# Kernel tuning notes

Measured on AMD Instinct MI355X. Metric: run time of the kernel, lower is better.

The kernel has to match this reference:

```python
import jax, jax.numpy as jnp
import numpy as np

N_HEADS = 32
N_KV_HEADS = 8


def _rope(x, cos, sin):
    # x: [B, S, H, D]; cos/sin: [S, D//2]; complex multiply on consecutive pairs
    B, S, H, D = x.shape
    xr = x.reshape(B, S, H, D // 2, 2)
    x0, x1 = xr[..., 0], xr[..., 1]
    c = cos[None, :, None, :]
    s = sin[None, :, None, :]
    o0 = x0 * c - x1 * s
    o1 = x0 * s + x1 * c
    return jnp.stack([o0, o1], axis=-1).reshape(B, S, H, D)


def setup_inputs():
    key = jax.random.key(0)
    ks = jax.random.split(key, 5)
    B, S, D = 1, 2048, 2048
    hd = D // N_HEADS  # 64
    x = jax.random.normal(ks[0], (B, S, D), jnp.float32)
    wq = jax.random.normal(ks[1], (D, D), jnp.float32) * 0.02
    wk = jax.random.normal(ks[2], (D, N_KV_HEADS * hd), jnp.float32) * 0.02
    wv = jax.random.normal(ks[3], (D, N_KV_HEADS * hd), jnp.float32) * 0.02
    wo = jax.random.normal(ks[4], (D, D), jnp.float32) * 0.02
    # true rotary frequencies (theta_cis = exp(i * pos * freq)), shape [S, hd//2]
    pos = jnp.arange(S, dtype=jnp.float32)
    freqs = 1.0 / (10000.0 ** (jnp.arange(0, hd, 2, dtype=jnp.float32) / hd))
    ang = pos[:, None] * freqs[None, :]
    return {"x": x, "theta_cos": jnp.cos(ang), "theta_sin": jnp.sin(ang),
            "wq": wq, "wk": wk, "wv": wv, "wo": wo}


def reference(x, theta_cos, theta_sin, wq, wk, wv, wo):
    B, S, D = x.shape
    hd = D // N_HEADS
    rep = N_HEADS // N_KV_HEADS
    xq = (x @ wq).reshape(B, S, N_HEADS, hd)
    # NOTE: module applies RoPE to K and V (not Q) - reproduced faithfully
    xk = _rope((x @ wk).reshape(B, S, N_KV_HEADS, hd), theta_cos, theta_sin)
    xv = _rope((x @ wv).reshape(B, S, N_KV_HEADS, hd), theta_cos, theta_sin)
    # GQA: repeat_interleave kv heads along head dim
    xk = jnp.repeat(xk, rep, axis=2)
    xv = jnp.repeat(xv, rep, axis=2)
    att = jnp.einsum('bqhd,bkhd->bhqk', xq, xk) * (hd ** -0.5)
    # faithful to torch.tril + masked_fill(att == 0.0, -inf)
    att = jnp.tril(att)
    att = jnp.where(att == 0.0, -jnp.inf, att)
    att = jax.nn.softmax(att, axis=-1)
    y = jnp.einsum('bhqk,bkhd->bqhd', att, xv).reshape(B, S, D)
    return y @ wo
```

## Files before the change

kernel.cpp:

```cpp
#include <hip/hip_runtime.h>

typedef unsigned short u16;
typedef unsigned int   u32;
typedef __bf16 bf16x8 __attribute__((ext_vector_type(8)));
typedef float  f32x4  __attribute__((ext_vector_type(4)));

__device__ __forceinline__ u16 f2bf(float f) {
    u32 x = __builtin_bit_cast(u32, f);
    x += 0x7fffu + ((x >> 16) & 1u);
    return (u16)(x >> 16);
}

__device__ __forceinline__ bf16x8 ld_frag(const u16* p) {
    return __builtin_bit_cast(bf16x8, *(const uint4*)p);
}

__device__ __forceinline__ f32x4 mfma16(bf16x8 a, bf16x8 b, f32x4 c) {
    return __builtin_amdgcn_mfma_f32_16x16x32_bf16(a, b, c, 0, 0, 0);
}

__device__ __forceinline__ void gl_lds16(const u16* g, u16* l) {
#if __has_builtin(__builtin_amdgcn_global_load_lds)
    __builtin_amdgcn_global_load_lds(
        (__attribute__((address_space(1))) const void*)g,
        (__attribute__((address_space(3))) void*)l, 16, 0, 0);
#else
    *(uint4*)l = *(const uint4*)g;
#endif
}

__global__ void f2b_vec(const float* __restrict__ in, u16* __restrict__ out, int n4) {
    int i = blockIdx.x * blockDim.x + threadIdx.x;
    if (i >= n4) return;
    float4 v = ((const float4*)in)[i];
    u32 a = (u32)f2bf(v.x) | ((u32)f2bf(v.y) << 16);
    u32 b = (u32)f2bf(v.z) | ((u32)f2bf(v.w) << 16);
    ((uint2*)out)[i] = make_uint2(a, b);
}

__global__ void transpose_f2b(const float* __restrict__ in, u16* __restrict__ out, int R, int C) {
    __shared__ float t[32][33];
    int c0 = blockIdx.x * 32, r0 = blockIdx.y * 32;
    for (int i = threadIdx.y; i < 32; i += 8)
        t[i][threadIdx.x] = in[(size_t)(r0 + i) * C + c0 + threadIdx.x];
    __syncthreads();
    for (int i = threadIdx.y; i < 32; i += 8)
        out[(size_t)(c0 + i) * R + r0 + threadIdx.x] = f2bf(t[threadIdx.x][i]);
}

__device__ __forceinline__ void gemm_core(const u16* __restrict__ A, const u16* __restrict__ BT,
                                          float* Cf, u16* Cb, int m0, int n0, int N, int K) {
    __shared__ __align__(16) u16 As[128 * 32];
    __shared__ __align__(16) u16 Bs[128 * 32];
    const int tid = threadIdx.x, wave = tid >> 6, lane = tid & 63;
    const int quad = lane >> 4, l15 = lane & 15;
    const int wr = wave >> 1, wc = wave & 1;
    f32x4 acc[4][4] = {};
    for (int k0 = 0; k0 < K; k0 += 32) {
        const u16* Ag = A + (size_t)m0 * K + k0;
        const u16* Bg = BT + (size_t)n0 * K + k0;
#pragma unroll
        for (int r2 = 0; r2 < 2; r2++) {
            int i = r2 * 256 + tid;
            gl_lds16(Ag + (size_t)(i >> 2) * K + (i & 3) * 8, &As[i * 8]);
            gl_lds16(Bg + (size_t)(i >> 2) * K + (i & 3) * 8, &Bs[i * 8]);
        }
        __syncthreads();
        bf16x8 af[4], bfr[4];
#pragma unroll
        for (int i = 0; i < 4; i++) {
            af[i]  = ld_frag(&As[(wr * 64 + i * 16 + l15) * 32 + quad * 8]);
            bfr[i] = ld_frag(&Bs[(wc * 64 + i * 16 + l15) * 32 + quad * 8]);
        }
#pragma unroll
        for (int i = 0; i < 4; i++)
#pragma unroll
            for (int j = 0; j < 4; j++)
                acc[i][j] = mfma16(af[i], bfr[j], acc[i][j]);
        __syncthreads();
    }
    if (Cb) {
#pragma unroll
        for (int i = 0; i < 4; i++)
#pragma unroll
            for (int r = 0; r < 4; r++) {
                u16* p = Cb + (size_t)(m0 + wr * 64 + i * 16 + quad * 4 + r) * N + n0 + wc * 64 + l15;
#pragma unroll
                for (int j = 0; j < 4; j++) p[j * 16] = f2bf(acc[i][j][r]);
            }
    } else {
#pragma unroll
        for (int i = 0; i < 4; i++)
#pragma unroll
            for (int r = 0; r < 4; r++) {
                float* p = Cf + (size_t)(m0 + wr * 64 + i * 16 + quad * 4 + r) * N + n0 + wc * 64 + l15;
#pragma unroll
                for (int j = 0; j < 4; j++) p[j * 16] = acc[i][j][r];
            }
    }
}

__global__ __launch_bounds__(256) void gemm_proj(const u16* __restrict__ A,
                                                 const u16* __restrict__ wqT,
                                                 const u16* __restrict__ wkT,
                                                 const u16* __restrict__ wvT,
                                                 u16* Qb, float* Kraw, float* Vraw) {
    int bx = blockIdx.x, m0 = blockIdx.y * 128;
    if (bx < 16)      gemm_core(A, wqT, nullptr, Qb, m0, bx * 128, 2048, 2048);
    else if (bx < 20) gemm_core(A, wkT, Kraw, nullptr, m0, (bx - 16) * 128, 512, 2048);
    else              gemm_core(A, wvT, Vraw, nullptr, m0, (bx - 20) * 128, 512, 2048);
}

__global__ __launch_bounds__(256) void gemm_out(const u16* __restrict__ A,
                                                const u16* __restrict__ BT,
                                                float* __restrict__ C) {
    gemm_core(A, BT, C, nullptr, blockIdx.y * 128, blockIdx.x * 128, 2048, 2048);
}

__global__ void rope_kernel(const float* __restrict__ Kraw, float* __restrict__ Vraw,
                            const float* __restrict__ cosb, const float* __restrict__ sinb,
                            u16* __restrict__ Kb) {
    int p = blockIdx.x * 256 + threadIdx.x;
    int s = p >> 8, rem = p & 255, t = rem & 31;
    float c = cosb[s * 32 + t], sn = sinb[s * 32 + t];
    float2 k2 = ((const float2*)Kraw)[p];
    float k0 = k2.x * c - k2.y * sn, k1 = k2.x * sn + k2.y * c;
    ((u32*)Kb)[p] = (u32)f2bf(k0) | ((u32)f2bf(k1) << 16);
    float2 v2 = ((const float2*)Vraw)[p];
    float2 o;
    o.x = v2.x * c - v2.y * sn;
    o.y = v2.x * sn + v2.y * c;
    ((float2*)Vraw)[p] = o;
}

#define LP 72
struct AttnSmem {
    u16 QPs[64 * LP];
    u16 Ks[64 * LP];
    u16 Vs[64 * LP];
};

__global__ __launch_bounds__(256) void attn_kernel(const u16* __restrict__ Qb,
                                                   const u16* __restrict__ Kb,
                                                   const u16* __restrict__ VbT,
                                                   u16* __restrict__ Yb,
                                                   float* __restrict__ Opart,
                                                   float* __restrict__ lpart) {
    __shared__ __align__(16) AttnSmem sm;
    const int tid = threadIdx.x, w = tid >> 6, lane = tid & 63;
    const int quad = lane >> 4, l15 = lane & 15;
    const int x = blockIdx.x, h = blockIdx.y, kvh = h >> 2;

    int qt, kvlo, kvhi, pt = 0;
    bool partial;
    if (x < 16) { qt = x; kvlo = 0; kvhi = x + 1; partial = false; }
    else {
        int t = 16 + ((x - 16) >> 1), sp = (x - 16) & 1;
        int nk = t + 1, a = (nk + 1) >> 1;
        qt = t; kvlo = sp ? a : 0; kvhi = sp ? nk : a; partial = true;
        pt = (t - 16) * 2 + sp;
    }
    const int q0 = qt * 64;

    const u16* Qg = Qb + (size_t)q0 * 2048 + h * 64;
#pragma unroll
    for (int r2 = 0; r2 < 2; r2++) {
        int i = r2 * 256 + tid, row = i >> 3, c8 = (i & 7) * 8;
        *(uint4*)&sm.QPs[row * LP + c8] = *(const uint4*)(Qg + (size_t)row * 2048 + c8);
    }
    __syncthreads();
    bf16x8 aQ0 = ld_frag(&sm.QPs[(w * 16 + l15) * LP + quad * 8]);
    bf16x8 aQ1 = ld_frag(&sm.QPs[(w * 16 + l15) * LP + 32 + quad * 8]);

    f32x4 O[4] = {};
    float l_acc[4] = {0.f, 0.f, 0.f, 0.f};
    u16* Ps = &sm.QPs[w * 16 * LP];

    for (int jt = kvlo; jt < kvhi; jt++) {
        const int j0 = jt * 64;
        __syncthreads();
        const u16* Kg = Kb + (size_t)j0 * 512 + kvh * 64;
        const u16* Vg = VbT + (size_t)(kvh * 64) * 2048 + j0;
#pragma unroll
        for (int r2 = 0; r2 < 2; r2++) {
            int i = r2 * 256 + tid, row = i >> 3, c8 = (i & 7) * 8;
            *(uint4*)&sm.Ks[row * LP + c8] = *(const uint4*)(Kg + (size_t)row * 512 + c8);
            *(uint4*)&sm.Vs[row * LP + c8] = *(const uint4*)(Vg + (size_t)row * 2048 + c8);
        }
        __syncthreads();

        f32x4 s[4];
#pragma unroll
        for (int j = 0; j < 4; j++) {
            bf16x8 b0 = ld_frag(&sm.Ks[(j * 16 + l15) * LP + quad * 8]);
            bf16x8 b1 = ld_frag(&sm.Ks[(j * 16 + l15) * LP + 32 + quad * 8]);
            f32x4 z = {};
            z = mfma16(aQ0, b0, z);
            z = mfma16(aQ1, b1, z);
            s[j] = z;
        }
        const bool diag = (jt == qt);
#pragma unroll
        for (int j = 0; j < 4; j++)
#pragma unroll
            for (int r = 0; r < 4; r++) {
                float p = __expf(s[j][r] * 0.125f);
                if (diag && (j * 16 + l15) > (w * 16 + quad * 4 + r)) p = 0.f;
                s[j][r] = p;
                l_acc[r] += p;
            }
#pragma unroll
        for (int j = 0; j < 4; j++)
#pragma unroll
            for (int r = 0; r < 4; r++)
                Ps[(quad * 4 + r) * LP + j * 16 + l15] = f2bf(s[j][r]);
        bf16x8 aP0 = ld_frag(&Ps[l15 * LP + quad * 8]);
        bf16x8 aP1 = ld_frag(&Ps[l15 * LP + 32 + quad * 8]);
#pragma unroll
        for (int j = 0; j < 4; j++) {
            bf16x8 v0 = ld_frag(&sm.Vs[(j * 16 + l15) * LP + quad * 8]);
            bf16x8 v1 = ld_frag(&sm.Vs[(j * 16 + l15) * LP + 32 + quad * 8]);
            O[j] = mfma16(aP0, v0, O[j]);
            O[j] = mfma16(aP1, v1, O[j]);
        }
    }
    float l_i[4];
#pragma unroll
    for (int r = 0; r < 4; r++) {
        float rs = l_acc[r];
        rs += __shfl_xor(rs, 1); rs += __shfl_xor(rs, 2);
        rs += __shfl_xor(rs, 4); rs += __shfl_xor(rs, 8);
        l_i[r] = rs;
    }
    if (!partial) {
#pragma unroll
        for (int r = 0; r < 4; r++) {
            float inv = __frcp_rn(l_i[r]);
#pragma unroll
            for (int j = 0; j < 4; j++)
                Yb[(size_t)(q0 + w * 16 + quad * 4 + r) * 2048 + h * 64 + j * 16 + l15] =
                    f2bf(O[j][r] * inv);
        }
    } else {
        float* Og = Opart + ((size_t)(pt * 32 + h) * 64) * 64;
#pragma unroll
        for (int r = 0; r < 4; r++) {
            int row = w * 16 + quad * 4 + r;
#pragma unroll
            for (int j = 0; j < 4; j++)
                Og[(size_t)row * 64 + j * 16 + l15] = O[j][r];
            if (l15 == 0) lpart[(size_t)(pt * 32 + h) * 64 + row] = l_i[r];
        }
    }
}

__global__ void combine_kernel(const float* __restrict__ Opart,
                               const float* __restrict__ lpart,
                               u16* __restrict__ Yb) {
    int e = blockIdx.x * 256 + threadIdx.x;
    int d4 = e & 15, h = (e >> 4) & 31, rg = e >> 9;
    int t16 = rg >> 6, row = rg & 63;
    int s0 = (t16 * 2) * 32 + h, s1 = s0 + 32;
    float4 a = ((const float4*)Opart)[((size_t)s0 * 64 + row) * 16 + d4];
    float4 b = ((const float4*)Opart)[((size_t)s1 * 64 + row) * 16 + d4];
    float l = lpart[(size_t)s0 * 64 + row] + lpart[(size_t)s1 * 64 + row];
    float inv = __frcp_rn(l);
    u32 lo = (u32)f2bf((a.x + b.x) * inv) | ((u32)f2bf((a.y + b.y) * inv) << 16);
    u32 hi = (u32)f2bf((a.z + b.z) * inv) | ((u32)f2bf((a.w + b.w) * inv) << 16);
    int q = 1024 + rg;
    ((uint2*)(Yb + (size_t)q * 2048 + h * 64))[d4] = make_uint2(lo, hi);
}

extern "C" void kernel_launch(void* const* d_in, const int* in_sizes, int n_in,
                              void* d_out, int out_size, void* d_ws, size_t ws_size,
                              hipStream_t stream) {
    const float* x  = (const float*)d_in[0];
    const float* tc = (const float*)d_in[1];
    const float* ts = (const float*)d_in[2];
    const float* wq = (const float*)d_in[3];
    const float* wk = (const float*)d_in[4];
    const float* wv = (const float*)d_in[5];
    const float* wo = (const float*)d_in[6];
    float* out = (float*)d_out;

    char* w = (char*)d_ws;
    u16*   xb   = (u16*)(w);
    u16*   wqT  = (u16*)(w + (8u  << 20));
    u16*   wkT  = (u16*)(w + (16u << 20));
    u16*   wvT  = (u16*)(w + (18u << 20));
    u16*   woT  = (u16*)(w + (20u << 20));
    u16*   Qb   = (u16*)(w + (28u << 20));
    float* Kraw = (float*)(w + (36u << 20));
    float* Vraw = (float*)(w + (40u << 20));
    u16*   Kb   = (u16*)(w + (44u << 20));
    u16*   VbT  = (u16*)(w + (46u << 20));
    u16*   Yb   = (u16*)(w + (36u << 20));
    float* Opart= (float*)(w);
    float* lpart= (float*)(w + (16u << 20));

    f2b_vec<<<4096, 256, 0, stream>>>(x, xb, 1048576);
    transpose_f2b<<<dim3(64, 64), dim3(32, 8), 0, stream>>>(wq, wqT, 2048, 2048);
    transpose_f2b<<<dim3(16, 64), dim3(32, 8), 0, stream>>>(wk, wkT, 2048, 512);
    transpose_f2b<<<dim3(16, 64), dim3(32, 8), 0, stream>>>(wv, wvT, 2048, 512);
    transpose_f2b<<<dim3(64, 64), dim3(32, 8), 0, stream>>>(wo, woT, 2048, 2048);
    gemm_proj<<<dim3(24, 16), 256, 0, stream>>>(xb, wqT, wkT, wvT, Qb, Kraw, Vraw);
    rope_kernel<<<2048, 256, 0, stream>>>(Kraw, Vraw, tc, ts, Kb);
    transpose_f2b<<<dim3(16, 64), dim3(32, 8), 0, stream>>>(Vraw, VbT, 2048, 512);
    attn_kernel<<<dim3(48, 32), 256, 0, stream>>>(Qb, Kb, VbT, Yb, Opart, lpart);
    combine_kernel<<<2048, 256, 0, stream>>>(Opart, lpart, Yb);
    gemm_out<<<dim3(16, 16), 256, 0, stream>>>(Yb, woT, out);
}
```

Measured before the change: 291.6 us.

## Split-K output GEMM, process two KV tiles per attention iteration, reorder attention task schedule

The output projection is split along K into two halves run as 512 blocks writing partial results, followed by a new kernel that sums them. This fills more CUs than the previous 256-block launch but adds an extra fp32 write and read pass. The attention kernel now processes 128 keys per loop iteration with wider shared-memory tiles. It also maps blocks through a task table that issues the longest query tiles first, for better load balancing. Workspace offsets are rearranged so the new partial buffers fit, which risks aliasing mistakes.

```diff
diff --git a/kernel.cpp b/kernel.cpp
--- a/kernel.cpp
+++ b/kernel.cpp
@@ -49,21 +49,22 @@
 }
 
 __device__ __forceinline__ void gemm_core(const u16* __restrict__ A, const u16* __restrict__ BT,
-                                          float* Cf, u16* Cb, int m0, int n0, int N, int K) {
+                                          float* Cf, u16* Cb, int m0, int n0, int N, int Kstride,
+                                          int ks, int ke) {
     __shared__ __align__(16) u16 As[128 * 32];
     __shared__ __align__(16) u16 Bs[128 * 32];
     const int tid = threadIdx.x, wave = tid >> 6, lane = tid & 63;
     const int quad = lane >> 4, l15 = lane & 15;
     const int wr = wave >> 1, wc = wave & 1;
     f32x4 acc[4][4] = {};
-    for (int k0 = 0; k0 < K; k0 += 32) {
-        const u16* Ag = A + (size_t)m0 * K + k0;
-        const u16* Bg = BT + (size_t)n0 * K + k0;
+    for (int k0 = ks; k0 < ke; k0 += 32) {
+        const u16* Ag = A + (size_t)m0 * Kstride + k0;
+        const u16* Bg = BT + (size_t)n0 * Kstride + k0;
 #pragma unroll
         for (int r2 = 0; r2 < 2; r2++) {
             int i = r2 * 256 + tid;
-            gl_lds16(Ag + (size_t)(i >> 2) * K + (i & 3) * 8, &As[i * 8]);
-            gl_lds16(Bg + (size_t)(i >> 2) * K + (i & 3) * 8, &Bs[i * 8]);
+            gl_lds16(Ag + (size_t)(i >> 2) * Kstride + (i & 3) * 8, &As[i * 8]);
+            gl_lds16(Bg + (size_t)(i >> 2) * Kstride + (i & 3) * 8, &Bs[i * 8]);
         }
         __syncthreads();
         bf16x8 af[4], bfr[4];
@@ -106,15 +107,25 @@
                                                  const u16* __restrict__ wvT,
                                                  u16* Qb, float* Kraw, float* Vraw) {
     int bx = blockIdx.x, m0 = blockIdx.y * 128;
-    if (bx < 16)      gemm_core(A, wqT, nullptr, Qb, m0, bx * 128, 2048, 2048);
-    else if (bx < 20) gemm_core(A, wkT, Kraw, nullptr, m0, (bx - 16) * 128, 512, 2048);
-    else              gemm_core(A, wvT, Vraw, nullptr, m0, (bx - 20) * 128, 512, 2048);
-}
-
-__global__ __launch_bounds__(256) void gemm_out(const u16* __restrict__ A,
-                                                const u16* __restrict__ BT,
-                                                float* __restrict__ C) {
-    gemm_core(A, BT, C, nullptr, blockIdx.y * 128, blockIdx.x * 128, 2048, 2048);
+    if (bx < 16)      gemm_core(A, wqT, nullptr, Qb, m0, bx * 128, 2048, 2048, 0, 2048);
+    else if (bx < 20) gemm_core(A, wkT, Kraw, nullptr, m0, (bx - 16) * 128, 512, 2048, 0, 2048);
+    else              gemm_core(A, wvT, Vraw, nullptr, m0, (bx - 20) * 128, 512, 2048, 0, 2048);
+}
+
+__global__ __launch_bounds__(256) void gemm_out_split(const u16* __restrict__ A,
+                                                      const u16* __restrict__ BT,
+                                                      float* __restrict__ Cpart) {
+    int z = blockIdx.z;
+    gemm_core(A, BT, Cpart + (size_t)z * 2048 * 2048, nullptr,
+              blockIdx.y * 128, blockIdx.x * 128, 2048, 2048, z * 1024, (z + 1) * 1024);
+}
+
+__global__ void combine_out(const float* __restrict__ Cpart, float* __restrict__ out) {
+    int i = blockIdx.x * 256 + threadIdx.x;
+    float4 a = ((const float4*)Cpart)[i];
+    float4 b = ((const float4*)(Cpart + 2048 * 2048))[i];
+    float4 o; o.x = a.x + b.x; o.y = a.y + b.y; o.z = a.z + b.z; o.w = a.w + b.w;
+    ((float4*)out)[i] = o;
 }
 
 __global__ void rope_kernel(const float* __restrict__ Kraw, float* __restrict__ Vraw,
@@ -133,11 +144,25 @@
     ((float2*)Vraw)[p] = o;
 }
 
-#define LP 72
+#define LPK 72
+#define LPV 136
+#define T_(q,l,h) (((u32)(q) << 16) | ((u32)(l) << 8) | (u32)(h))
+__device__ const u32 ATASK[48] = {
+    T_(14,0,15), T_(15,0,16), T_(28,0,16), T_(29,0,16), T_(30,0,16), T_(31,0,16), T_(30,16,31), T_(31,16,32),
+    T_(12,0,13), T_(13,0,14), T_(24,0,14), T_(25,0,14), T_(26,0,14), T_(27,0,14), T_(26,14,27), T_(27,14,28),
+    T_(28,16,29), T_(29,16,30),
+    T_(10,0,11), T_(11,0,12), T_(20,0,12), T_(21,0,12), T_(22,0,12), T_(23,0,12), T_(22,12,23), T_(23,12,24),
+    T_(24,14,25), T_(25,14,26),
+    T_(8,0,9), T_(9,0,10), T_(16,0,10), T_(17,0,10), T_(18,0,10), T_(19,0,10), T_(18,10,19), T_(19,10,20),
+    T_(20,12,21), T_(21,12,22),
+    T_(6,0,7), T_(7,0,8), T_(16,10,17), T_(17,10,18),
+    T_(4,0,5), T_(5,0,6), T_(2,0,3), T_(3,0,4), T_(0,0,1), T_(1,0,2)
+};
+
 struct AttnSmem {
-    u16 QPs[64 * LP];
-    u16 Ks[64 * LP];
-    u16 Vs[64 * LP];
+    u16 Ks[128 * LPK];
+    u16 Vs[64 * LPV];
+    u16 QPs[4 * 16 * LPV];
 };
 
 __global__ __launch_bounds__(256) void attn_kernel(const u16* __restrict__ Qb,
@@ -149,80 +174,79 @@
     __shared__ __align__(16) AttnSmem sm;
     const int tid = threadIdx.x, w = tid >> 6, lane = tid & 63;
     const int quad = lane >> 4, l15 = lane & 15;
-    const int x = blockIdx.x, h = blockIdx.y, kvh = h >> 2;
-
-    int qt, kvlo, kvhi, pt = 0;
-    bool partial;
-    if (x < 16) { qt = x; kvlo = 0; kvhi = x + 1; partial = false; }
-    else {
-        int t = 16 + ((x - 16) >> 1), sp = (x - 16) & 1;
-        int nk = t + 1, a = (nk + 1) >> 1;
-        qt = t; kvlo = sp ? a : 0; kvhi = sp ? nk : a; partial = true;
-        pt = (t - 16) * 2 + sp;
-    }
+    const int h = blockIdx.x, kvh = h >> 2;
+    const u32 tk = ATASK[blockIdx.y];
+    const int qt = tk >> 16, lo = (tk >> 8) & 255, hi = tk & 255;
+    const bool partial = (qt >= 16);
+    const int pt = partial ? ((qt - 16) * 2 + (lo != 0)) : 0;
     const int q0 = qt * 64;
 
     const u16* Qg = Qb + (size_t)q0 * 2048 + h * 64;
 #pragma unroll
     for (int r2 = 0; r2 < 2; r2++) {
         int i = r2 * 256 + tid, row = i >> 3, c8 = (i & 7) * 8;
-        *(uint4*)&sm.QPs[row * LP + c8] = *(const uint4*)(Qg + (size_t)row * 2048 + c8);
+        *(uint4*)&sm.QPs[row * LPK + c8] = *(const uint4*)(Qg + (size_t)row * 2048 + c8);
     }
     __syncthreads();
-    bf16x8 aQ0 = ld_frag(&sm.QPs[(w * 16 + l15) * LP + quad * 8]);
-    bf16x8 aQ1 = ld_frag(&sm.QPs[(w * 16 + l15) * LP + 32 + quad * 8]);
+    bf16x8 aQ0 = ld_frag(&sm.QPs[(w * 16 + l15) * LPK + quad * 8]);
+    bf16x8 aQ1 = ld_frag(&sm.QPs[(w * 16 + l15) * LPK + 32 + quad * 8]);
 
     f32x4 O[4] = {};
     float l_acc[4] = {0.f, 0.f, 0.f, 0.f};
-    u16* Ps = &sm.QPs[w * 16 * LP];
-
-    for (int jt = kvlo; jt < kvhi; jt++) {
+    u16* Ps = &sm.QPs[w * 16 * LPV];
+    const int qrow = q0 + w * 16 + quad * 4;
+
+    for (int jt = lo; jt < hi; jt += 2) {
         const int j0 = jt * 64;
         __syncthreads();
         const u16* Kg = Kb + (size_t)j0 * 512 + kvh * 64;
         const u16* Vg = VbT + (size_t)(kvh * 64) * 2048 + j0;
 #pragma unroll
-        for (int r2 = 0; r2 < 2; r2++) {
-            int i = r2 * 256 + tid, row = i >> 3, c8 = (i & 7) * 8;
-            *(uint4*)&sm.Ks[row * LP + c8] = *(const uint4*)(Kg + (size_t)row * 512 + c8);
-            *(uint4*)&sm.Vs[row * LP + c8] = *(const uint4*)(Vg + (size_t)row * 2048 + c8);
+        for (int r2 = 0; r2 < 4; r2++) {
+            int i = r2 * 256 + tid;
+            int krow = i >> 3, kc = (i & 7) * 8;
+            *(uint4*)&sm.Ks[krow * LPK + kc] = *(const uint4*)(Kg + (size_t)krow * 512 + kc);
+            int vrow = i >> 4, vc = (i & 15) * 8;
+            *(uint4*)&sm.Vs[vrow * LPV + vc] = *(const uint4*)(Vg + (size_t)vrow * 2048 + vc);
         }
         __syncthreads();
 
-        f32x4 s[4];
-#pragma unroll
-        for (int j = 0; j < 4; j++) {
-            bf16x8 b0 = ld_frag(&sm.Ks[(j * 16 + l15) * LP + quad * 8]);
-            bf16x8 b1 = ld_frag(&sm.Ks[(j * 16 + l15) * LP + 32 + quad * 8]);
+        f32x4 s[8];
+#pragma unroll
+        for (int j = 0; j < 8; j++) {
+            bf16x8 b0 = ld_frag(&sm.Ks[(j * 16 + l15) * LPK + quad * 8]);
+            bf16x8 b1 = ld_frag(&sm.Ks[(j * 16 + l15) * LPK + 32 + quad * 8]);
             f32x4 z = {};
             z = mfma16(aQ0, b0, z);
             z = mfma16(aQ1, b1, z);
             s[j] = z;
         }
-        const bool diag = (jt == qt);
-#pragma unroll
-        for (int j = 0; j < 4; j++)
+        const bool needmask = (jt + 1) >= qt;
+#pragma unroll
+        for (int j = 0; j < 8; j++)
 #pragma unroll
             for (int r = 0; r < 4; r++) {
                 float p = __expf(s[j][r] * 0.125f);
-                if (diag && (j * 16 + l15) > (w * 16 + quad * 4 + r)) p = 0.f;
+                if (needmask && (j0 + j * 16 + l15) > (qrow + r)) p = 0.f;
                 s[j][r] = p;
                 l_acc[r] += p;
             }
 #pragma unroll
+        for (int j = 0; j < 8; j++)
+#pragma unroll
+            for (int r = 0; r < 4; r++)
+                Ps[(quad * 4 + r) * LPV + j * 16 + l15] = f2bf(s[j][r]);
+        bf16x8 aP[4];
+#pragma unroll
+        for (int kk = 0; kk < 4; kk++)
+            aP[kk] = ld_frag(&Ps[l15 * LPV + kk * 32 + quad * 8]);
+#pragma unroll
         for (int j = 0; j < 4; j++)
 #pragma unroll
-            for (int r = 0; r < 4; r++)
-                Ps[(quad * 4 + r) * LP + j * 16 + l15] = f2bf(s[j][r]);
-        bf16x8 aP0 = ld_frag(&Ps[l15 * LP + quad * 8]);
-        bf16x8 aP1 = ld_frag(&Ps[l15 * LP + 32 + quad * 8]);
-#pragma unroll
-        for (int j = 0; j < 4; j++) {
-            bf16x8 v0 = ld_frag(&sm.Vs[(j * 16 + l15) * LP + quad * 8]);
-            bf16x8 v1 = ld_frag(&sm.Vs[(j * 16 + l15) * LP + 32 + quad * 8]);
-            O[j] = mfma16(aP0, v0, O[j]);
-            O[j] = mfma16(aP1, v1, O[j]);
-        }
+            for (int kk = 0; kk < 4; kk++) {
+                bf16x8 v = ld_frag(&sm.Vs[(j * 16 + l15) * LPV + kk * 32 + quad * 8]);
+                O[j] = mfma16(aP[kk], v, O[j]);
+            }
     }
     float l_i[4];
 #pragma unroll
@@ -285,18 +309,19 @@
 
     char* w = (char*)d_ws;
     u16*   xb   = (u16*)(w);
-    u16*   wqT  = (u16*)(w + (8u  << 20));
+    u16*   Yb   = (u16*)(w);
+    u16*   woT  = (u16*)(w + (8u  << 20));
     u16*   wkT  = (u16*)(w + (16u << 20));
     u16*   wvT  = (u16*)(w + (18u << 20));
-    u16*   woT  = (u16*)(w + (20u << 20));
-    u16*   Qb   = (u16*)(w + (28u << 20));
-    float* Kraw = (float*)(w + (36u << 20));
-    float* Vraw = (float*)(w + (40u << 20));
-    u16*   Kb   = (u16*)(w + (44u << 20));
-    u16*   VbT  = (u16*)(w + (46u << 20));
-    u16*   Yb   = (u16*)(w + (36u << 20));
-    float* Opart= (float*)(w);
-    float* lpart= (float*)(w + (16u << 20));
+    u16*   wqT  = (u16*)(w + (20u << 20));
+    float* Kraw = (float*)(w + (28u << 20));
+    float* Vraw = (float*)(w + (32u << 20));
+    u16*   Kb   = (u16*)(w + (36u << 20));
+    u16*   VbT  = (u16*)(w + (38u << 20));
+    u16*   Qb   = (u16*)(w + (40u << 20));
+    float* Opart= (float*)(w + (16u << 20));
+    float* lpart= (float*)(w + (32u << 20));
+    float* Cpart= (float*)(w + (16u << 20));
 
     f2b_vec<<<4096, 256, 0, stream>>>(x, xb, 1048576);
     transpose_f2b<<<dim3(64, 64), dim3(32, 8), 0, stream>>>(wq, wqT, 2048, 2048);
@@ -306,7 +331,8 @@
     gemm_proj<<<dim3(24, 16), 256, 0, stream>>>(xb, wqT, wkT, wvT, Qb, Kraw, Vraw);
     rope_kernel<<<2048, 256, 0, stream>>>(Kraw, Vraw, tc, ts, Kb);
     transpose_f2b<<<dim3(16, 64), dim3(32, 8), 0, stream>>>(Vraw, VbT, 2048, 512);
-    attn_kernel<<<dim3(48, 32), 256, 0, stream>>>(Qb, Kb, VbT, Yb, Opart, lpart);
+    attn_kernel<<<dim3(32, 48), 256, 0, stream>>>(Qb, Kb, VbT, Yb, Opart, lpart);
     combine_kernel<<<2048, 256, 0, stream>>>(Opart, lpart, Yb);
-    gemm_out<<<dim3(16, 16), 256, 0, stream>>>(Yb, woT, out);
-}
+    gemm_out_split<<<dim3(16, 16, 2), 256, 0, stream>>>(Yb, woT, Cpart);
+    combine_out<<<4096, 256, 0, stream>>>(Cpart, out);
+}
```

Result: faster. 280.0 us (-4.0%).
